# Kernel optimization log

Hardware: AMD Instinct MI355X
Metric: run time of the kernel (lower is better)

The kernel has to match this reference:

```python
import jax, jax.numpy as jnp
import numpy as np

NUM_TOKENS = 16384
DIM = 4096
N_EXPERTS = 256
ROUTE_SCALE = 1.0


def setup_inputs() -> dict:
    key = jax.random.key(0)
    k_x, k_w = jax.random.split(key)
    x = jax.random.normal(k_x, (NUM_TOKENS, DIM), dtype=jnp.float32)
    # nn.init.normal_(weight, std=0.02)
    weight = 0.02 * jax.random.normal(k_w, (N_EXPERTS, DIM), dtype=jnp.float32)
    return {"x": x, "weight": weight}


def reference(x, weight):
    # Router GEMM: [T, D] @ [D, E] -> [T, E]
    scores = jnp.einsum("td,ed->te", x, weight)
    # Eval-mode token_choice path: softmax in fp32
    probs = jax.nn.softmax(scores.astype(jnp.float32), axis=-1)  # [T, E]
    indices = jnp.argmax(probs, axis=-1, keepdims=True)  # [T, 1] int
    # Hard one-hot scatter of argmax
    y_hard = jax.nn.one_hot(indices[:, 0], N_EXPERTS, dtype=probs.dtype)  # [T, E]
    # Straight-through estimator mix
    ste = jax.lax.stop_gradient(y_hard - probs) + probs
    # Gather routing weight at the selected expert
    weights = jnp.take_along_axis(ste, indices, axis=-1)  # [T, 1]
    weights = (weights * ROUTE_SCALE).astype(x.dtype)
    return weights, indices
```

## Files before the change

### kernel.cpp

```cpp
#include <hip/hip_runtime.h>
#include <stdint.h>

#define NUM_TOKENS 16384
#define DIM        4096
#define NEXP       256
#define MB         32
#define BK         64
#define NITER      (DIM / BK)
#define APAD       72
#define NWAVES     8
#define MARGIN     0.025f
#define CAP        16384

typedef __attribute__((ext_vector_type(4))) float   f32x4;
typedef __attribute__((ext_vector_type(8))) __bf16  bf16x8;

static __device__ __forceinline__ unsigned short f32_to_bf16(float f) {
    unsigned int u = __float_as_uint(f);
    u += 0x7fffu + ((u >> 16) & 1u);
    return (unsigned short)(u >> 16);
}

__global__ void cvt_weights(const float* __restrict__ w,
                            unsigned short* __restrict__ wh,
                            int* __restrict__ counter) {
    if (blockIdx.x == 0 && threadIdx.x == 0) *counter = 0;
    const int n4 = NEXP * DIM / 4;
    const int stride = gridDim.x * blockDim.x;
    for (int i = blockIdx.x * blockDim.x + threadIdx.x; i < n4; i += stride) {
        float4 v = ((const float4*)w)[i];
        ushort4 h;
        h.x = f32_to_bf16(v.x); h.y = f32_to_bf16(v.y);
        h.z = f32_to_bf16(v.z); h.w = f32_to_bf16(v.w);
        ((ushort4*)wh)[i] = h;
    }
}

__global__ __launch_bounds__(512, 4) void gate_main(
    const float* __restrict__ x,
    const unsigned short* __restrict__ wh,
    float* __restrict__ out,
    int* __restrict__ counter,
    int4* __restrict__ entries)
{
    __shared__ unsigned short lAh[2][MB][APAD];
    __shared__ unsigned short lBh[2][NEXP * BK];
    __shared__ float4 cand[NWAVES][MB];

    const int tid  = threadIdx.x;
    const int wv   = tid >> 6;
    const int lane = tid & 63;
    const int tok0 = blockIdx.x * MB;

    const int ta   = tid >> 4;
    const int kcol = (tid & 15) * 4;
    const float* xrow = x + (size_t)(tok0 + ta) * DIM + kcol;

    const int esub   = lane >> 3;
    const int bk_off = ((lane & 7) ^ esub) * 8;

    const int quad = lane >> 4;
    const int col  = lane & 15;

    f32x4 acc[2][2];
    #pragma unroll
    for (int mt = 0; mt < 2; ++mt)
        #pragma unroll
        for (int nt = 0; nt < 2; ++nt)
            acc[mt][nt] = f32x4{0.f, 0.f, 0.f, 0.f};

    auto stage_b = [&](int it, int buf) {
        const int k0 = it * BK;
        #pragma unroll
        for (int jj = 0; jj < 4; ++jj) {
            const int e = wv * 32 + jj * 8 + esub;
            const unsigned short* gh = wh + (size_t)e * DIM + k0 + bk_off;
            unsigned short* dh = &lBh[buf][(wv * 32 + jj * 8) * BK];
            __builtin_amdgcn_global_load_lds(
                (const __attribute__((address_space(1))) unsigned int*)gh,
                (__attribute__((address_space(3))) unsigned int*)dh, 16, 0, 0);
        }
    };

    float4 xv = *(const float4*)(xrow);
    stage_b(0, 0);
    {
        ushort4 h;
        h.x = f32_to_bf16(xv.x); h.y = f32_to_bf16(xv.y);
        h.z = f32_to_bf16(xv.z); h.w = f32_to_bf16(xv.w);
        *(ushort4*)&lAh[0][ta][kcol] = h;
    }
    xv = *(const float4*)(xrow + BK);

    for (int it = 0; it < NITER; ++it) {
        const int cur = it & 1;
        const int nxt = cur ^ 1;

        if (it + 1 < NITER) {
            stage_b(it + 1, nxt);
            asm volatile("s_waitcnt vmcnt(5) lgkmcnt(0)" ::: "memory");
        } else {
            asm volatile("s_waitcnt vmcnt(0) lgkmcnt(0)" ::: "memory");
        }
        __builtin_amdgcn_s_barrier();
        asm volatile("" ::: "memory");

        if (it + 1 < NITER) {
            ushort4 h;
            h.x = f32_to_bf16(xv.x); h.y = f32_to_bf16(xv.y);
            h.z = f32_to_bf16(xv.z); h.w = f32_to_bf16(xv.w);
            *(ushort4*)&lAh[nxt][ta][kcol] = h;
            if (it + 2 < NITER)
                xv = *(const float4*)(xrow + (it + 2) * BK);
        }

        #pragma unroll
        for (int kk = 0; kk < BK; kk += 32) {
            const int kc = kk >> 3;
            bf16x8 ah[2], bh[2];
            #pragma unroll
            for (int mt = 0; mt < 2; ++mt)
                ah[mt] = *(const bf16x8*)&lAh[cur][mt * 16 + col][kk + quad * 8];
            #pragma unroll
            for (int nt = 0; nt < 2; ++nt) {
                const int e = wv * 32 + nt * 16 + col;
                const int cpos = (((kc + quad) ^ (col & 7)) * 8);
                bh[nt] = *(const bf16x8*)&lBh[cur][e * BK + cpos];
            }
            #pragma unroll
            for (int mt = 0; mt < 2; ++mt)
                #pragma unroll
                for (int nt = 0; nt < 2; ++nt)
                    acc[mt][nt] = __builtin_amdgcn_mfma_f32_16x16x32_bf16(
                        ah[mt], bh[nt], acc[mt][nt], 0, 0, 0);
        }

        asm volatile("" ::: "memory");
        __builtin_amdgcn_s_barrier();
        asm volatile("" ::: "memory");
    }

    #pragma unroll
    for (int mt = 0; mt < 2; ++mt) {
        #pragma unroll
        for (int r = 0; r < 4; ++r) {
            float s0 = acc[mt][0][r]; int e0 = wv * 32 + col;
            float s1 = acc[mt][1][r]; int e1 = e0 + 16;
            float t1s, t2s; int t1e, t2e;
            if (s1 > s0) { t1s = s1; t1e = e1; t2s = s0; t2e = e0; }
            else         { t1s = s0; t1e = e0; t2s = s1; t2e = e1; }
            #pragma unroll
            for (int m = 1; m <= 8; m <<= 1) {
                float o1s = __shfl_xor(t1s, m); int o1e = __shfl_xor(t1e, m);
                float o2s = __shfl_xor(t2s, m); int o2e = __shfl_xor(t2e, m);
                bool o1_top = (o1s > t1s) || (o1s == t1s && o1e < t1e);
                if (o1_top) {
                    bool keep_t1 = (t1s > o2s) || (t1s == o2s && t1e < o2e);
                    t2s = keep_t1 ? t1s : o2s; t2e = keep_t1 ? t1e : o2e;
                    t1s = o1s; t1e = o1e;
                } else {
                    bool o1_2nd = (o1s > t2s) || (o1s == t2s && o1e < t2e);
                    if (o1_2nd) { t2s = o1s; t2e = o1e; }
                }
            }
            if (col == 0) {
                int tok = mt * 16 + quad * 4 + r;
                cand[wv][tok] = make_float4(t1s, __int_as_float(t1e), t2s, __int_as_float(t2e));
            }
        }
    }
    __syncthreads();

    if (tid < MB) {
        float4 c0 = cand[0][tid];
        float t1s = c0.x; int t1e = __float_as_int(c0.y);
        float t2s = c0.z; int t2e = __float_as_int(c0.w);
        #pragma unroll
        for (int wvi = 1; wvi < NWAVES; ++wvi) {
            float4 c = cand[wvi][tid];
            float o1s = c.x; int o1e = __float_as_int(c.y);
            float o2s = c.z; int o2e = __float_as_int(c.w);
            bool o1_top = (o1s > t1s) || (o1s == t1s && o1e < t1e);
            if (o1_top) {
                bool keep_t1 = (t1s > o2s) || (t1s == o2s && t1e < o2e);
                t2s = keep_t1 ? t1s : o2s; t2e = keep_t1 ? t1e : o2e;
                t1s = o1s; t1e = o1e;
            } else {
                bool o1_2nd = (o1s > t2s) || (o1s == t2s && o1e < t2e);
                if (o1_2nd) { t2s = o1s; t2e = o1e; }
            }
        }
        const int gtok = tok0 + tid;
        out[gtok] = 1.0f;
        out[NUM_TOKENS + gtok] = (float)t1e;
        if (t1s - t2s < MARGIN) {
            int slot = atomicAdd(counter, 1);
            if (slot < CAP) entries[slot] = make_int4(gtok, t1e, t2e, 0);
        }
    }
}

__global__ void refine(const float* __restrict__ x,
                       const float* __restrict__ w,
                       const int* __restrict__ counter,
                       const int4* __restrict__ entries,
                       float* __restrict__ out) {
    const int gwave  = (blockIdx.x * blockDim.x + threadIdx.x) >> 6;
    const int lane   = threadIdx.x & 63;
    const int nwaves = (gridDim.x * blockDim.x) >> 6;
    int n = *counter; if (n > CAP) n = CAP;
    for (int i = gwave; i < n; i += nwaves) {
        int4 e = entries[i];
        const float* xr = x + (size_t)e.x * DIM;
        const float* w1 = w + (size_t)e.y * DIM;
        const float* w2 = w + (size_t)e.z * DIM;
        double d1 = 0.0, d2 = 0.0;
        for (int k = lane; k < DIM; k += 64) {
            double xv = (double)xr[k];
            d1 += xv * (double)w1[k];
            d2 += xv * (double)w2[k];
        }
        #pragma unroll
        for (int m = 32; m > 0; m >>= 1) {
            d1 += __shfl_xor(d1, m);
            d2 += __shfl_xor(d2, m);
        }
        if (lane == 0) {
            int best = (d1 > d2) ? e.y : ((d2 > d1) ? e.z : (e.y < e.z ? e.y : e.z));
            out[NUM_TOKENS + e.x] = (float)best;
        }
    }
}

extern "C" void kernel_launch(void* const* d_in, const int* in_sizes, int n_in,
                              void* d_out, int out_size, void* d_ws, size_t ws_size,
                              hipStream_t stream) {
    const float* x = (const float*)d_in[0];
    const float* w = (const float*)d_in[1];
    float* out = (float*)d_out;

    char* ws = (char*)d_ws;
    unsigned short* wh = (unsigned short*)ws;
    int*  counter = (int*)(ws + (2u << 20));
    int4* entries = (int4*)(ws + (2u << 20) + 16);

    cvt_weights<<<256, 256, 0, stream>>>(w, wh, counter);
    gate_main<<<NUM_TOKENS / MB, 512, 0, stream>>>(x, wh, out, counter, entries);
    refine<<<256, 256, 0, stream>>>(x, w, counter, entries, out);
}
```

Measured before the change: 434.0 us.

## Load router weight fragments directly into registers instead of staging through LDS

The bf16 weight tile no longer goes through shared memory via global_load_lds. Each wave now loads its B fragments straight from global memory into registers, one k-step ahead. The x staging is made three-deep and the loop is unrolled by two with ping-pong buffers, leaving a single barrier per iteration. This cuts LDS traffic and footprint, which may raise occupancy, but relies on L2/L1 to serve the per-lane uncoalesced 16-byte weight loads, and load latency is now exposed in registers.

```diff
diff --git a/kernel.cpp b/kernel.cpp
--- a/kernel.cpp
+++ b/kernel.cpp
@@ -44,7 +44,6 @@
     int4* __restrict__ entries)
 {
     __shared__ unsigned short lAh[2][MB][APAD];
-    __shared__ unsigned short lBh[2][NEXP * BK];
     __shared__ float4 cand[NWAVES][MB];
 
     const int tid  = threadIdx.x;
@@ -56,12 +55,14 @@
     const int kcol = (tid & 15) * 4;
     const float* xrow = x + (size_t)(tok0 + ta) * DIM + kcol;
 
-    const int esub   = lane >> 3;
-    const int bk_off = ((lane & 7) ^ esub) * 8;
-
     const int quad = lane >> 4;
     const int col  = lane & 15;
 
+    const unsigned short* bp[2];
+    #pragma unroll
+    for (int nt = 0; nt < 2; ++nt)
+        bp[nt] = wh + (size_t)(wv * 32 + nt * 16 + col) * DIM + quad * 8;
+
     f32x4 acc[2][2];
     #pragma unroll
     for (int mt = 0; mt < 2; ++mt)
@@ -69,75 +70,60 @@
         for (int nt = 0; nt < 2; ++nt)
             acc[mt][nt] = f32x4{0.f, 0.f, 0.f, 0.f};
 
-    auto stage_b = [&](int it, int buf) {
-        const int k0 = it * BK;
-        #pragma unroll
-        for (int jj = 0; jj < 4; ++jj) {
-            const int e = wv * 32 + jj * 8 + esub;
-            const unsigned short* gh = wh + (size_t)e * DIM + k0 + bk_off;
-            unsigned short* dh = &lBh[buf][(wv * 32 + jj * 8) * BK];
-            __builtin_amdgcn_global_load_lds(
-                (const __attribute__((address_space(1))) unsigned int*)gh,
-                (__attribute__((address_space(3))) unsigned int*)dh, 16, 0, 0);
-        }
-    };
-
-    float4 xv = *(const float4*)(xrow);
-    stage_b(0, 0);
+    bf16x8 b[2][2];
+
+    float4 xva = *(const float4*)(xrow);
+    float4 xvb = *(const float4*)(xrow + BK);
+    #pragma unroll
+    for (int kk2 = 0; kk2 < 2; ++kk2)
+        #pragma unroll
+        for (int nt = 0; nt < 2; ++nt)
+            b[kk2][nt] = *(const bf16x8*)(bp[nt] + kk2 * 32);
     {
         ushort4 h;
-        h.x = f32_to_bf16(xv.x); h.y = f32_to_bf16(xv.y);
-        h.z = f32_to_bf16(xv.z); h.w = f32_to_bf16(xv.w);
+        h.x = f32_to_bf16(xva.x); h.y = f32_to_bf16(xva.y);
+        h.z = f32_to_bf16(xva.z); h.w = f32_to_bf16(xva.w);
         *(ushort4*)&lAh[0][ta][kcol] = h;
     }
-    xv = *(const float4*)(xrow + BK);
-
-    for (int it = 0; it < NITER; ++it) {
-        const int cur = it & 1;
+    xva = *(const float4*)(xrow + 2 * BK);
+
+    asm volatile("s_waitcnt lgkmcnt(0)" ::: "memory");
+    __builtin_amdgcn_s_barrier();
+    asm volatile("" ::: "memory");
+
+    auto iter_body = [&](int it, int cur, float4& xcons) {
         const int nxt = cur ^ 1;
-
         if (it + 1 < NITER) {
-            stage_b(it + 1, nxt);
-            asm volatile("s_waitcnt vmcnt(5) lgkmcnt(0)" ::: "memory");
-        } else {
-            asm volatile("s_waitcnt vmcnt(0) lgkmcnt(0)" ::: "memory");
-        }
+            ushort4 h;
+            h.x = f32_to_bf16(xcons.x); h.y = f32_to_bf16(xcons.y);
+            h.z = f32_to_bf16(xcons.z); h.w = f32_to_bf16(xcons.w);
+            *(ushort4*)&lAh[nxt][ta][kcol] = h;
+            if (it + 3 < NITER)
+                xcons = *(const float4*)(xrow + (it + 3) * BK);
+        }
+        #pragma unroll
+        for (int kk2 = 0; kk2 < 2; ++kk2) {
+            bf16x8 ah0 = *(const bf16x8*)&lAh[cur][col][kk2 * 32 + quad * 8];
+            bf16x8 ah1 = *(const bf16x8*)&lAh[cur][16 + col][kk2 * 32 + quad * 8];
+            acc[0][0] = __builtin_amdgcn_mfma_f32_16x16x32_bf16(ah0, b[kk2][0], acc[0][0], 0, 0, 0);
+            acc[1][0] = __builtin_amdgcn_mfma_f32_16x16x32_bf16(ah1, b[kk2][0], acc[1][0], 0, 0, 0);
+            acc[0][1] = __builtin_amdgcn_mfma_f32_16x16x32_bf16(ah0, b[kk2][1], acc[0][1], 0, 0, 0);
+            acc[1][1] = __builtin_amdgcn_mfma_f32_16x16x32_bf16(ah1, b[kk2][1], acc[1][1], 0, 0, 0);
+            if (it + 1 < NITER) {
+                #pragma unroll
+                for (int nt = 0; nt < 2; ++nt)
+                    b[kk2][nt] = *(const bf16x8*)(bp[nt] + (it + 1) * BK + kk2 * 32);
+            }
+        }
+        asm volatile("s_waitcnt lgkmcnt(0)" ::: "memory");
         __builtin_amdgcn_s_barrier();
         asm volatile("" ::: "memory");
-
-        if (it + 1 < NITER) {
-            ushort4 h;
-            h.x = f32_to_bf16(xv.x); h.y = f32_to_bf16(xv.y);
-            h.z = f32_to_bf16(xv.z); h.w = f32_to_bf16(xv.w);
-            *(ushort4*)&lAh[nxt][ta][kcol] = h;
-            if (it + 2 < NITER)
-                xv = *(const float4*)(xrow + (it + 2) * BK);
-        }
-
-        #pragma unroll
-        for (int kk = 0; kk < BK; kk += 32) {
-            const int kc = kk >> 3;
-            bf16x8 ah[2], bh[2];
-            #pragma unroll
-            for (int mt = 0; mt < 2; ++mt)
-                ah[mt] = *(const bf16x8*)&lAh[cur][mt * 16 + col][kk + quad * 8];
-            #pragma unroll
-            for (int nt = 0; nt < 2; ++nt) {
-                const int e = wv * 32 + nt * 16 + col;
-                const int cpos = (((kc + quad) ^ (col & 7)) * 8);
-                bh[nt] = *(const bf16x8*)&lBh[cur][e * BK + cpos];
-            }
-            #pragma unroll
-            for (int mt = 0; mt < 2; ++mt)
-                #pragma unroll
-                for (int nt = 0; nt < 2; ++nt)
-                    acc[mt][nt] = __builtin_amdgcn_mfma_f32_16x16x32_bf16(
-                        ah[mt], bh[nt], acc[mt][nt], 0, 0, 0);
-        }
-
-        asm volatile("" ::: "memory");
-        __builtin_amdgcn_s_barrier();
-        asm volatile("" ::: "memory");
+    };
+
+    #pragma unroll 1
+    for (int itp = 0; itp < NITER; itp += 2) {
+        iter_body(itp,     0, xvb);
+        iter_body(itp + 1, 1, xva);
     }
 
     #pragma unroll
```

New measurement: 456.4 us. 1.05x slower.
